# Kernel optimization log

Hardware: AMD Instinct MI355X
Metric: run time of the kernel (lower is better)

Reference implementation:

```python
import jax, jax.numpy as jnp
import numpy as np
from jax import lax

K = 5          # kernel_size
P = K // 2     # padding
DN = ('NCHW', 'OIHW', 'NCHW')


def _dwconv(z, wt, bt):
    # depthwise conv: z [b,c,h,w], wt [c,1,K,K], bt [c]
    c = z.shape[1]
    y = lax.conv_general_dilated(z, wt, (1, 1), [(P, P), (P, P)],
                                 feature_group_count=c, dimension_numbers=DN)
    return y + bt[None, :, None, None]


def setup_inputs() -> dict:
    key = jax.random.key(0)
    ks = jax.random.split(key, 8)
    b, c, h, w = 8, 64, 256, 256
    return {
        'x': jax.random.normal(ks[0], (b, c, h, w), jnp.float32),
        'w1': jax.random.normal(ks[1], (3, c, 1, K, K), jnp.float32) * 0.1,
        'b1': jax.random.normal(ks[2], (3, c), jnp.float32) * 0.1,
        'w2': jax.random.normal(ks[3], (3, c, 1, K, K), jnp.float32) * 0.1,
        'b2': jax.random.normal(ks[4], (3, c), jnp.float32) * 0.1,
        'wk': jax.random.normal(ks[5], (K * K * c, c), jnp.float32) * 0.1,
        'bk': jax.random.normal(ks[6], (K * K * c,), jnp.float32) * 0.1,
        'bias': jnp.zeros((c,), jnp.float32),
    }


def reference(x, w1, b1, w2, b2, wk, bk, bias):
    b, c, h, w = x.shape
    # avgpool 2x2 stride 2
    t = x.reshape(b, c, h // 2, 2, w // 2, 2).mean(axis=(3, 5))
    # Block1: 3 depthwise convs
    for i in range(3):
        t = _dwconv(t, w1[i], b1[i])
    # maxpool 2x2 stride 2
    hh, ww = t.shape[2], t.shape[3]
    t = t.reshape(b, c, hh // 2, 2, ww // 2, 2).max(axis=(3, 5))
    # Block2: 3 depthwise convs
    for i in range(3):
        t = _dwconv(t, w2[i], b2[i])
    # adaptive avg pool to 1x1 -> [b, c]
    g = t.mean(axis=(2, 3))
    # tokernel 1x1 conv -> per-sample depthwise kernels [b*c, 1, K, K]
    kern = (jnp.einsum('bc,oc->bo', g, wk) + bk).reshape(b * c, 1, K, K)
    # per-sample dynamic depthwise conv (groups = b*c)
    y = lax.conv_general_dilated(x.reshape(1, b * c, h, w), kern, (1, 1),
                                 [(P, P), (P, P)], feature_group_count=b * c,
                                 dimension_numbers=DN)
    return y.reshape(b, c, h, w) + bias[None, :, None, None]
```

## Files before the change

### kernel.cpp

```cpp
#include <hip/hip_runtime.h>

#define BB 8
#define CC 64
#define HH 256
#define WW 256
#define KK 5

template<int SS>
__device__ __forceinline__ void conv4x4_e12(const float* __restrict__ src,
                                            const float* __restrict__ wr,
                                            float bv, float a[4][4])
{
#pragma unroll
    for (int i = 0; i < 4; i++)
#pragma unroll
        for (int j = 0; j < 4; j++) a[i][j] = bv;
#pragma unroll
    for (int ir = 0; ir < 8; ir++) {
        const float* s = src + ir * SS;
        float4 A = *(const float4*)s;
        float4 B = *(const float4*)(s + 4);
        float4 C = *(const float4*)(s + 8);
        float e[12] = {A.x, A.y, A.z, A.w, B.x, B.y, B.z, B.w, C.x, C.y, C.z, C.w};
#pragma unroll
        for (int i = 0; i < 4; i++) {
            const int ky = ir - i;
            if (ky >= 0 && ky < 5) {
#pragma unroll
                for (int kx = 0; kx < 5; kx++) {
                    const float wv = wr[ky * 5 + kx];
#pragma unroll
                    for (int j = 0; j < 4; j++) a[i][j] += e[2 + j + kx] * wv;
                }
            }
        }
    }
}

template<int SS>
__device__ __forceinline__ void conv2x4_e12(const float* __restrict__ src,
                                            const float* __restrict__ wr,
                                            float bv, float a[2][4])
{
#pragma unroll
    for (int i = 0; i < 2; i++)
#pragma unroll
        for (int j = 0; j < 4; j++) a[i][j] = bv;
#pragma unroll
    for (int ir = 0; ir < 6; ir++) {
        const float* s = src + ir * SS;
        float4 A = *(const float4*)s;
        float4 B = *(const float4*)(s + 4);
        float4 C = *(const float4*)(s + 8);
        float e[12] = {A.x, A.y, A.z, A.w, B.x, B.y, B.z, B.w, C.x, C.y, C.z, C.w};
#pragma unroll
        for (int i = 0; i < 2; i++) {
            const int ky = ir - i;
            if (ky >= 0 && ky < 5) {
#pragma unroll
                for (int kx = 0; kx < 5; kx++) {
                    const float wv = wr[ky * 5 + kx];
#pragma unroll
                    for (int j = 0; j < 4; j++) a[i][j] += e[2 + j + kx] * wv;
                }
            }
        }
    }
}

__global__ __launch_bounds__(640, 8) void k_a1(
    const float* __restrict__ x, const float* __restrict__ w1,
    const float* __restrict__ b1, float* __restrict__ t2)
{
    const int plane = blockIdx.x;
    const int c = plane & 63;
    const int by = blockIdx.y;
    const int R0 = by * 64;
    const int tid = threadIdx.x;

    __shared__ __align__(16) float sb[76 * 160];

    const float* xp = x + (size_t)plane * HH * WW;

#pragma unroll
    for (int k = 0; k < 5; k++) {
        int i = tid + k * 640;
        if (i < 76 * 36) {
            int r = i / 36, q = i % 36;
            int pr = R0 - 6 + r;
            float4 v = make_float4(0.f, 0.f, 0.f, 0.f);
            if (q >= 2 && q <= 33 && (unsigned)pr < 128u) {
                int xc = 8 * q - 16;
                const float* p0 = xp + (size_t)(2 * pr) * WW + xc;
                const float* p1 = p0 + WW;
                float4 a0 = *(const float4*)p0;
                float4 a1 = *(const float4*)(p0 + 4);
                float4 b0 = *(const float4*)p1;
                float4 b1v = *(const float4*)(p1 + 4);
                v.x = 0.25f * (a0.x + a0.y + b0.x + b0.y);
                v.y = 0.25f * (a0.z + a0.w + b0.z + b0.w);
                v.z = 0.25f * (a1.x + a1.y + b1v.x + b1v.y);
                v.w = 0.25f * (a1.z + a1.w + b1v.z + b1v.w);
            }
            *(float4*)&sb[r * 160 + 4 * q] = v;
        }
    }
    __syncthreads();

    const int v = tid / 34, u = tid % 34;

    {
        float wr[25];
#pragma unroll
        for (int k = 0; k < 25; k++) wr[k] = w1[0 * CC * 25 + c * 25 + k];
        const float bv = b1[0 * CC + c];
        float a[4][4];
        const bool act = tid < 612;
        if (act) {
            conv4x4_e12<160>(&sb[(4 * v) * 160 + 4 * u], wr, bv, a);
            const bool cok = (u >= 1 && u <= 32);
#pragma unroll
            for (int i = 0; i < 4; i++) {
                int gi = R0 - 4 + 4 * v + i;
                bool ok = cok && ((unsigned)gi < 128u);
#pragma unroll
                for (int j = 0; j < 4; j++) if (!ok) a[i][j] = 0.f;
            }
        }
        __syncthreads();
        if (act) {
#pragma unroll
            for (int i = 0; i < 4; i++)
                *(float4*)&sb[(4 * v + 2 + i) * 160 + 4 * u + 4] =
                    make_float4(a[i][0], a[i][1], a[i][2], a[i][3]);
        }
        __syncthreads();
    }

    {
        float wr[25];
#pragma unroll
        for (int k = 0; k < 25; k++) wr[k] = w1[1 * CC * 25 + c * 25 + k];
        const float bv = b1[1 * CC + c];
        float a[4][4];
        const bool act = tid < 578;
        if (act) {
            conv4x4_e12<160>(&sb[(2 + 4 * v) * 160 + 4 * u], wr, bv, a);
            const bool cok = (u >= 1 && u <= 32);
#pragma unroll
            for (int i = 0; i < 4; i++) {
                int gi = R0 - 2 + 4 * v + i;
                bool ok = cok && ((unsigned)gi < 128u);
#pragma unroll
                for (int j = 0; j < 4; j++) if (!ok) a[i][j] = 0.f;
            }
        }
        __syncthreads();
        if (act) {
#pragma unroll
            for (int i = 0; i < 4; i++)
                *(float4*)&sb[(4 + 4 * v + i) * 160 + 4 * u + 4] =
                    make_float4(a[i][0], a[i][1], a[i][2], a[i][3]);
        }
        __syncthreads();
    }

    {
        float wr[25];
#pragma unroll
        for (int k = 0; k < 25; k++) wr[k] = w1[2 * CC * 25 + c * 25 + k];
        const float bv = b1[2 * CC + c];
        if (tid < 544) {
            float a[4][4];
            conv4x4_e12<160>(&sb[(4 + 4 * v) * 160 + 4 * u], wr, bv, a);
            if (u >= 1 && u <= 32) {
                const int pr0 = (R0 >> 1) + 2 * v;
                const int pc0 = 2 * u - 2;
#pragma unroll
                for (int ii = 0; ii < 2; ii++) {
                    float m0 = fmaxf(fmaxf(a[2 * ii][0], a[2 * ii][1]),
                                     fmaxf(a[2 * ii + 1][0], a[2 * ii + 1][1]));
                    float m1 = fmaxf(fmaxf(a[2 * ii][2], a[2 * ii][3]),
                                     fmaxf(a[2 * ii + 1][2], a[2 * ii + 1][3]));
                    *(float2*)&t2[((size_t)plane * 64 + pr0 + ii) * 64 + pc0] =
                        make_float2(m0, m1);
                }
            }
        }
    }
}

__global__ __launch_bounds__(512, 4) void k_b(
    const float* __restrict__ t2, const float* __restrict__ w2,
    const float* __restrict__ b2, float* __restrict__ g)
{
    const int plane = blockIdx.x;
    const int c = plane & 63;
    const int tid = threadIdx.x;

    __shared__ __align__(16) float sb[68 * 72];
    __shared__ float red[8];

    const float* tp = t2 + (size_t)plane * 4096;

#pragma unroll
    for (int k = 0; k < 3; k++) {
        int i = tid + k * 512;
        if (i < 68 * 18) {
            int r = i / 18, q = i % 18;
            float4 v = make_float4(0.f, 0.f, 0.f, 0.f);
            if (r >= 2 && r < 66 && q >= 1 && q <= 16)
                v = *(const float4*)(tp + (size_t)(r - 2) * 64 + 4 * (q - 1));
            *(float4*)&sb[r * 72 + 4 * q] = v;
        }
    }
    __syncthreads();

    const int v = tid >> 4, u = tid & 15;
    const float* rb = &sb[(2 * v) * 72 + 4 * u];
    float* wb = &sb[(2 * v + 2) * 72 + 4 * u + 4];

#pragma unroll
    for (int cv = 0; cv < 2; cv++) {
        float wr[25];
#pragma unroll
        for (int k = 0; k < 25; k++) wr[k] = w2[cv * CC * 25 + c * 25 + k];
        float a[2][4];
        conv2x4_e12<72>(rb, wr, b2[cv * CC + c], a);
        __syncthreads();
#pragma unroll
        for (int i = 0; i < 2; i++)
            *(float4*)(wb + i * 72) = make_float4(a[i][0], a[i][1], a[i][2], a[i][3]);
        __syncthreads();
    }

    float s;
    {
        float wr[25];
#pragma unroll
        for (int k = 0; k < 25; k++) wr[k] = w2[2 * CC * 25 + c * 25 + k];
        float a[2][4];
        conv2x4_e12<72>(rb, wr, b2[2 * CC + c], a);
        s = (a[0][0] + a[0][1] + a[0][2] + a[0][3]) +
            (a[1][0] + a[1][1] + a[1][2] + a[1][3]);
    }
#pragma unroll
    for (int off = 32; off > 0; off >>= 1) s += __shfl_down(s, off);
    if ((tid & 63) == 0) red[tid >> 6] = s;
    __syncthreads();
    if (tid == 0) {
        float t = 0.f;
#pragma unroll
        for (int k = 0; k < 8; k++) t += red[k];
        g[plane] = t * (1.f / 4096.f);
    }
}

__global__ __launch_bounds__(256) void k_kern(
    const float* __restrict__ g, const float* __restrict__ wk,
    const float* __restrict__ bk, float* __restrict__ kern)
{
    const int o = blockIdx.x * 256 + threadIdx.x;
    const int b = o / 1600, oo = o - b * 1600;
    float v = bk[oo];
    const float* wp = wk + (size_t)oo * 64;
    const float* gp = g + b * 64;
#pragma unroll 16
    for (int k = 0; k < 64; k++) v += gp[k] * wp[k];
    kern[o] = v;
}

__global__ __launch_bounds__(256) void k_dyn(
    const float* __restrict__ x, const float* __restrict__ kern,
    const float* __restrict__ bias, float* __restrict__ out)
{
    const int plane = blockIdx.z;
    const int tx = blockIdx.x, ty = blockIdx.y;
    const int tid = threadIdx.x;

    __shared__ __align__(16) float sx[68 * 76];

    const float* xp = x + (size_t)plane * HH * WW;
    const int R0 = ty * 64, C0 = tx * 64;

#pragma unroll
    for (int k = 0; k < 5; k++) {
        int i = tid + k * 256;
        if (i < 68 * 18) {
            int r = i / 18, q = i - r * 18;
            int gr = R0 - 2 + r;
            int gc = C0 - 4 + 4 * q;
            float4 v = make_float4(0.f, 0.f, 0.f, 0.f);
            if ((unsigned)gr < HH && (unsigned)gc < WW)
                v = *(const float4*)(xp + (size_t)gr * WW + gc);
            *(float4*)&sx[r * 76 + 4 * q] = v;
        }
    }

    float w[25];
#pragma unroll
    for (int k = 0; k < 25; k++) w[k] = kern[(size_t)plane * 25 + k];
    const float bv = bias[plane & 63];

    __syncthreads();

    const int tr = (tid >> 4) * 4;
    const int tc = (tid & 15) * 4;
    float acc[4][4];
#pragma unroll
    for (int i = 0; i < 4; i++)
#pragma unroll
        for (int j = 0; j < 4; j++) acc[i][j] = bv;

#pragma unroll
    for (int ir = 0; ir < 8; ir++) {
        const float* s = &sx[(tr + ir) * 76 + tc];
        float4 A = *(const float4*)s;
        float4 B4 = *(const float4*)(s + 4);
        float4 Cv = *(const float4*)(s + 8);
        float e[12] = {A.x, A.y, A.z, A.w, B4.x, B4.y, B4.z, B4.w,
                       Cv.x, Cv.y, Cv.z, Cv.w};
#pragma unroll
        for (int i = 0; i < 4; i++) {
            const int ky = ir - i;
            if (ky >= 0 && ky < 5) {
#pragma unroll
                for (int kx = 0; kx < 5; kx++) {
                    const float wv = w[ky * 5 + kx];
#pragma unroll
                    for (int j = 0; j < 4; j++) acc[i][j] += e[j + kx + 2] * wv;
                }
            }
        }
    }

    float* op = out + (size_t)plane * HH * WW + (size_t)(R0 + tr) * WW + C0 + tc;
#pragma unroll
    for (int i = 0; i < 4; i++)
        *(float4*)(op + (size_t)i * WW) = make_float4(acc[i][0], acc[i][1], acc[i][2], acc[i][3]);
}

extern "C" void kernel_launch(void* const* d_in, const int* in_sizes, int n_in,
                              void* d_out, int out_size, void* d_ws, size_t ws_size,
                              hipStream_t stream)
{
    const float* x    = (const float*)d_in[0];
    const float* w1   = (const float*)d_in[1];
    const float* b1   = (const float*)d_in[2];
    const float* w2   = (const float*)d_in[3];
    const float* b2   = (const float*)d_in[4];
    const float* wk   = (const float*)d_in[5];
    const float* bk   = (const float*)d_in[6];
    const float* bias = (const float*)d_in[7];
    float* out = (float*)d_out;

    float* ws   = (float*)d_ws;
    float* t2   = ws;
    float* g    = ws + 2097152;
    float* kern = g + 512;

    k_a1<<<dim3(512, 2), 640, 0, stream>>>(x, w1, b1, t2);
    k_b<<<dim3(512), 512, 0, stream>>>(t2, w2, b2, g);
    k_kern<<<dim3(50), 256, 0, stream>>>(g, wk, bk, kern);
    k_dyn<<<dim3(4, 4, 512), 256, 0, stream>>>(x, kern, bias, out);
}
```

Before: 129.5 us.

## Retile fused avgpool+dwconv stage into 64x64 column tiles with 4x8 register blocking

Replaces the first fused kernel (avgpool, three depthwise convs, maxpool) with a version that also splits the width into two 64-column tiles, uses 256-thread blocks, and computes 4x8 outputs per thread instead of 4x4. Shared memory rows are XOR-swizzled in float4 units to reduce bank conflicts, and the final stage writes float4 results. The intent is more blocks with smaller shared footprint for better occupancy and more register reuse per loaded row. The cost is extra halo recomputation at the column split, and many threads sit idle during the conv stages (only 162, 153 and 128 of 256 are active).

```diff
diff --git a/kernel.cpp b/kernel.cpp
--- a/kernel.cpp
+++ b/kernel.cpp
@@ -6,32 +6,207 @@
 #define WW 256
 #define KK 5
 
-template<int SS>
-__device__ __forceinline__ void conv4x4_e12(const float* __restrict__ src,
-                                            const float* __restrict__ wr,
-                                            float bv, float a[4][4])
-{
-#pragma unroll
-    for (int i = 0; i < 4; i++)
-#pragma unroll
-        for (int j = 0; j < 4; j++) a[i][j] = bv;
-#pragma unroll
-    for (int ir = 0; ir < 8; ir++) {
-        const float* s = src + ir * SS;
-        float4 A = *(const float4*)s;
-        float4 B = *(const float4*)(s + 4);
-        float4 C = *(const float4*)(s + 8);
-        float e[12] = {A.x, A.y, A.z, A.w, B.x, B.y, B.z, B.w, C.x, C.y, C.z, C.w};
-#pragma unroll
-        for (int i = 0; i < 4; i++) {
-            const int ky = ir - i;
-            if (ky >= 0 && ky < 5) {
-#pragma unroll
-                for (int kx = 0; kx < 5; kx++) {
-                    const float wv = wr[ky * 5 + kx];
-#pragma unroll
-                    for (int j = 0; j < 4; j++) a[i][j] += e[2 + j + kx] * wv;
-                }
+__device__ __forceinline__ void load_e16(const float* __restrict__ sb,
+                                         int r, int sbase, float e[16])
+{
+    const int bit = (r >> 2) & 1;
+    const float* row = sb + r * 84;
+#pragma unroll
+    for (int m = 0; m < 4; m++) {
+        float4 t = *(const float4*)(row + 4 * ((sbase + m) ^ bit));
+        e[4 * m + 0] = t.x; e[4 * m + 1] = t.y;
+        e[4 * m + 2] = t.z; e[4 * m + 3] = t.w;
+    }
+}
+
+__global__ __launch_bounds__(256, 6) void k_a(
+    const float* __restrict__ x, const float* __restrict__ w1,
+    const float* __restrict__ b1, float* __restrict__ t2)
+{
+    const int plane = blockIdx.x;
+    const int c = plane & 63;
+    const int R0 = blockIdx.y * 64;
+    const int C0 = blockIdx.z * 64;
+    const int tid = threadIdx.x;
+
+    __shared__ __align__(16) float sb[76 * 84];
+
+    const float* xp = x + (size_t)plane * HH * WW;
+
+#pragma unroll
+    for (int k = 0; k < 12; k++) {
+        int i = tid + k * 256;
+        if (i < 76 * 40) {
+            int r = i / 40, j = i % 40;
+            int pr = R0 - 6 + r;
+            int ic = C0 + 2 * j - 8;
+            float2 v = make_float2(0.f, 0.f);
+            if ((unsigned)pr < 128u && (unsigned)ic < 128u) {
+                const float* p0 = xp + (size_t)(2 * pr) * WW + 2 * ic;
+                float4 a0 = *(const float4*)p0;
+                float4 a1 = *(const float4*)(p0 + WW);
+                v.x = 0.25f * (a0.x + a0.y + a1.x + a1.y);
+                v.y = 0.25f * (a0.z + a0.w + a1.z + a1.w);
+            }
+            int dd = (2 * j) ^ (((r >> 2) & 1) << 2);
+            *(float2*)&sb[r * 84 + dd] = v;
+        }
+    }
+    __syncthreads();
+
+    {
+        float wr[25];
+#pragma unroll
+        for (int k = 0; k < 25; k++) wr[k] = w1[0 * CC * 25 + c * 25 + k];
+        const float bv = b1[0 * CC + c];
+        const bool act = tid < 162;
+        const int v = tid / 9, u = tid % 9;
+        float a[4][8];
+#pragma unroll
+        for (int i = 0; i < 4; i++)
+#pragma unroll
+            for (int j = 0; j < 8; j++) a[i][j] = bv;
+        if (act) {
+#pragma unroll
+            for (int ir = 0; ir < 8; ir++) {
+                float e[16];
+                load_e16(sb, 4 * v + ir, 2 * u, e);
+#pragma unroll
+                for (int i = 0; i < 4; i++) {
+                    const int ky = ir - i;
+                    if (ky >= 0 && ky < 5) {
+#pragma unroll
+                        for (int kx = 0; kx < 5; kx++) {
+                            const float wv = wr[ky * 5 + kx];
+#pragma unroll
+                            for (int j = 0; j < 8; j++) a[i][j] += e[2 + j + kx] * wv;
+                        }
+                    }
+                }
+            }
+#pragma unroll
+            for (int i = 0; i < 4; i++) {
+                int gi = R0 - 4 + 4 * v + i;
+                bool rok = (unsigned)gi < 128u;
+#pragma unroll
+                for (int j = 0; j < 8; j++) {
+                    int ic = C0 + 8 * u - 4 + j;
+                    if (!(rok && (unsigned)ic < 128u)) a[i][j] = 0.f;
+                }
+            }
+        }
+        __syncthreads();
+        if (act) {
+#pragma unroll
+            for (int i = 0; i < 4; i++) {
+                const int rw = 4 * v + 2 + i;
+                const int bit = (rw >> 2) & 1;
+                float* row = sb + rw * 84;
+                *(float4*)(row + 4 * ((2 * u + 1) ^ bit)) =
+                    make_float4(a[i][0], a[i][1], a[i][2], a[i][3]);
+                *(float4*)(row + 4 * ((2 * u + 2) ^ bit)) =
+                    make_float4(a[i][4], a[i][5], a[i][6], a[i][7]);
+            }
+        }
+        __syncthreads();
+    }
+
+    {
+        float wr[25];
+#pragma unroll
+        for (int k = 0; k < 25; k++) wr[k] = w1[1 * CC * 25 + c * 25 + k];
+        const float bv = b1[1 * CC + c];
+        const bool act = tid < 153;
+        const int v = tid / 9, u = tid % 9;
+        float a[4][8];
+#pragma unroll
+        for (int i = 0; i < 4; i++)
+#pragma unroll
+            for (int j = 0; j < 8; j++) a[i][j] = bv;
+        if (act) {
+#pragma unroll
+            for (int ir = 0; ir < 8; ir++) {
+                float e[16];
+                load_e16(sb, 4 * v + 2 + ir, 2 * u, e);
+#pragma unroll
+                for (int i = 0; i < 4; i++) {
+                    const int ky = ir - i;
+                    if (ky >= 0 && ky < 5) {
+#pragma unroll
+                        for (int kx = 0; kx < 5; kx++) {
+                            const float wv = wr[ky * 5 + kx];
+#pragma unroll
+                            for (int j = 0; j < 8; j++) a[i][j] += e[2 + j + kx] * wv;
+                        }
+                    }
+                }
+            }
+#pragma unroll
+            for (int i = 0; i < 4; i++) {
+                int gi = R0 - 2 + 4 * v + i;
+                bool rok = (unsigned)gi < 128u;
+#pragma unroll
+                for (int j = 0; j < 8; j++) {
+                    int ic = C0 + 8 * u - 4 + j;
+                    if (!(rok && (unsigned)ic < 128u)) a[i][j] = 0.f;
+                }
+            }
+        }
+        __syncthreads();
+        if (act) {
+#pragma unroll
+            for (int i = 0; i < 4; i++) {
+                const int rw = 4 * v + 4 + i;
+                const int bit = (rw >> 2) & 1;
+                float* row = sb + rw * 84;
+                *(float4*)(row + 4 * ((2 * u + 1) ^ bit)) =
+                    make_float4(a[i][0], a[i][1], a[i][2], a[i][3]);
+                *(float4*)(row + 4 * ((2 * u + 2) ^ bit)) =
+                    make_float4(a[i][4], a[i][5], a[i][6], a[i][7]);
+            }
+        }
+        __syncthreads();
+    }
+
+    {
+        float wr[25];
+#pragma unroll
+        for (int k = 0; k < 25; k++) wr[k] = w1[2 * CC * 25 + c * 25 + k];
+        const float bv = b1[2 * CC + c];
+        if (tid < 128) {
+            const int v = tid >> 3, u = tid & 7;
+            float a[4][8];
+#pragma unroll
+            for (int i = 0; i < 4; i++)
+#pragma unroll
+                for (int j = 0; j < 8; j++) a[i][j] = bv;
+#pragma unroll
+            for (int ir = 0; ir < 8; ir++) {
+                float e[16];
+                load_e16(sb, 4 * v + 4 + ir, 2 * u + 1, e);
+#pragma unroll
+                for (int i = 0; i < 4; i++) {
+                    const int ky = ir - i;
+                    if (ky >= 0 && ky < 5) {
+#pragma unroll
+                        for (int kx = 0; kx < 5; kx++) {
+                            const float wv = wr[ky * 5 + kx];
+#pragma unroll
+                            for (int j = 0; j < 8; j++) a[i][j] += e[2 + j + kx] * wv;
+                        }
+                    }
+                }
+            }
+            const int PR0 = (R0 >> 1) + 2 * v;
+            const int PC0 = (C0 >> 1) + 4 * u;
+#pragma unroll
+            for (int ii = 0; ii < 2; ii++) {
+                float4 o;
+                o.x = fmaxf(fmaxf(a[2*ii][0], a[2*ii][1]), fmaxf(a[2*ii+1][0], a[2*ii+1][1]));
+                o.y = fmaxf(fmaxf(a[2*ii][2], a[2*ii][3]), fmaxf(a[2*ii+1][2], a[2*ii+1][3]));
+                o.z = fmaxf(fmaxf(a[2*ii][4], a[2*ii][5]), fmaxf(a[2*ii+1][4], a[2*ii+1][5]));
+                o.w = fmaxf(fmaxf(a[2*ii][6], a[2*ii][7]), fmaxf(a[2*ii+1][6], a[2*ii+1][7]));
+                *(float4*)&t2[((size_t)plane * 64 + PR0 + ii) * 64 + PC0] = o;
             }
         }
     }
@@ -62,128 +237,6 @@
                     const float wv = wr[ky * 5 + kx];
 #pragma unroll
                     for (int j = 0; j < 4; j++) a[i][j] += e[2 + j + kx] * wv;
-                }
-            }
-        }
-    }
-}
-
-__global__ __launch_bounds__(640, 8) void k_a1(
-    const float* __restrict__ x, const float* __restrict__ w1,
-    const float* __restrict__ b1, float* __restrict__ t2)
-{
-    const int plane = blockIdx.x;
-    const int c = plane & 63;
-    const int by = blockIdx.y;
-    const int R0 = by * 64;
-    const int tid = threadIdx.x;
-
-    __shared__ __align__(16) float sb[76 * 160];
-
-    const float* xp = x + (size_t)plane * HH * WW;
-
-#pragma unroll
-    for (int k = 0; k < 5; k++) {
-        int i = tid + k * 640;
-        if (i < 76 * 36) {
-            int r = i / 36, q = i % 36;
-            int pr = R0 - 6 + r;
-            float4 v = make_float4(0.f, 0.f, 0.f, 0.f);
-            if (q >= 2 && q <= 33 && (unsigned)pr < 128u) {
-                int xc = 8 * q - 16;
-                const float* p0 = xp + (size_t)(2 * pr) * WW + xc;
-                const float* p1 = p0 + WW;
-                float4 a0 = *(const float4*)p0;
-                float4 a1 = *(const float4*)(p0 + 4);
-                float4 b0 = *(const float4*)p1;
-                float4 b1v = *(const float4*)(p1 + 4);
-                v.x = 0.25f * (a0.x + a0.y + b0.x + b0.y);
-                v.y = 0.25f * (a0.z + a0.w + b0.z + b0.w);
-                v.z = 0.25f * (a1.x + a1.y + b1v.x + b1v.y);
-                v.w = 0.25f * (a1.z + a1.w + b1v.z + b1v.w);
-            }
-            *(float4*)&sb[r * 160 + 4 * q] = v;
-        }
-    }
-    __syncthreads();
-
-    const int v = tid / 34, u = tid % 34;
-
-    {
-        float wr[25];
-#pragma unroll
-        for (int k = 0; k < 25; k++) wr[k] = w1[0 * CC * 25 + c * 25 + k];
-        const float bv = b1[0 * CC + c];
-        float a[4][4];
-        const bool act = tid < 612;
-        if (act) {
-            conv4x4_e12<160>(&sb[(4 * v) * 160 + 4 * u], wr, bv, a);
-            const bool cok = (u >= 1 && u <= 32);
-#pragma unroll
-            for (int i = 0; i < 4; i++) {
-                int gi = R0 - 4 + 4 * v + i;
-                bool ok = cok && ((unsigned)gi < 128u);
-#pragma unroll
-                for (int j = 0; j < 4; j++) if (!ok) a[i][j] = 0.f;
-            }
-        }
-        __syncthreads();
-        if (act) {
-#pragma unroll
-            for (int i = 0; i < 4; i++)
-                *(float4*)&sb[(4 * v + 2 + i) * 160 + 4 * u + 4] =
-                    make_float4(a[i][0], a[i][1], a[i][2], a[i][3]);
-        }
-        __syncthreads();
-    }
-
-    {
-        float wr[25];
-#pragma unroll
-        for (int k = 0; k < 25; k++) wr[k] = w1[1 * CC * 25 + c * 25 + k];
-        const float bv = b1[1 * CC + c];
-        float a[4][4];
-        const bool act = tid < 578;
-        if (act) {
-            conv4x4_e12<160>(&sb[(2 + 4 * v) * 160 + 4 * u], wr, bv, a);
-            const bool cok = (u >= 1 && u <= 32);
-#pragma unroll
-            for (int i = 0; i < 4; i++) {
-                int gi = R0 - 2 + 4 * v + i;
-                bool ok = cok && ((unsigned)gi < 128u);
-#pragma unroll
-                for (int j = 0; j < 4; j++) if (!ok) a[i][j] = 0.f;
-            }
-        }
-        __syncthreads();
-        if (act) {
-#pragma unroll
-            for (int i = 0; i < 4; i++)
-                *(float4*)&sb[(4 + 4 * v + i) * 160 + 4 * u + 4] =
-                    make_float4(a[i][0], a[i][1], a[i][2], a[i][3]);
-        }
-        __syncthreads();
-    }
-
-    {
-        float wr[25];
-#pragma unroll
-        for (int k = 0; k < 25; k++) wr[k] = w1[2 * CC * 25 + c * 25 + k];
-        const float bv = b1[2 * CC + c];
-        if (tid < 544) {
-            float a[4][4];
-            conv4x4_e12<160>(&sb[(4 + 4 * v) * 160 + 4 * u], wr, bv, a);
-            if (u >= 1 && u <= 32) {
-                const int pr0 = (R0 >> 1) + 2 * v;
-                const int pc0 = 2 * u - 2;
-#pragma unroll
-                for (int ii = 0; ii < 2; ii++) {
-                    float m0 = fmaxf(fmaxf(a[2 * ii][0], a[2 * ii][1]),
-                                     fmaxf(a[2 * ii + 1][0], a[2 * ii + 1][1]));
-                    float m1 = fmaxf(fmaxf(a[2 * ii][2], a[2 * ii][3]),
-                                     fmaxf(a[2 * ii + 1][2], a[2 * ii + 1][3]));
-                    *(float2*)&t2[((size_t)plane * 64 + pr0 + ii) * 64 + pc0] =
-                        make_float2(m0, m1);
                 }
             }
         }
@@ -359,7 +412,7 @@
     float* g    = ws + 2097152;
     float* kern = g + 512;
 
-    k_a1<<<dim3(512, 2), 640, 0, stream>>>(x, w1, b1, t2);
+    k_a<<<dim3(512, 2, 2), 256, 0, stream>>>(x, w1, b1, t2);
     k_b<<<dim3(512), 512, 0, stream>>>(t2, w2, b2, g);
     k_kern<<<dim3(50), 256, 0, stream>>>(g, wk, bk, kern);
     k_dyn<<<dim3(4, 4, 512), 256, 0, stream>>>(x, kern, bias, out);
```

Result: slower. 136.9 us (+5.7%).
